# Performance work log

Hardware: AMD Instinct MI355X
Metric: run time of the kernel (lower is better)

The kernel has to match this reference:

```python
import jax, jax.numpy as jnp
import numpy as np

N_NODES = 50000


def gcn_conv(x, src, dst, W, b, n_nodes):
    """PyG GCNConv: add self-loops, sym-normalize, aggregate, linear.
    x' = D^{-1/2} (A + I) D^{-1/2} X W + b
    """
    loop = jnp.arange(n_nodes, dtype=src.dtype)
    s = jnp.concatenate([src, loop])  # [E + N]
    d = jnp.concatenate([dst, loop])
    h = x @ W  # [N, out]
    deg = jax.ops.segment_sum(jnp.ones_like(d, dtype=h.dtype), d, num_segments=n_nodes)
    dinv = jnp.where(deg > 0, jax.lax.rsqrt(deg), 0.0)
    norm = dinv[s] * dinv[d]  # [E + N]
    msg = h[s] * norm[:, None]  # gather + scale (edge-level, memory bound)
    out = jax.ops.segment_sum(msg, d, num_segments=n_nodes)
    return out + b


def setup_inputs() -> dict:
    key = jax.random.key(0)
    k1, k2, k3, k4 = jax.random.split(key, 4)
    n, e, d_in, d_hid, d_out = N_NODES, 800000, 128, 128, 64
    x = jax.random.normal(k1, (n, d_in), dtype=jnp.float32)
    edge_index = jax.random.randint(k2, (2, e), 0, n, dtype=jnp.int64)
    W1 = jax.random.normal(k3, (d_in, d_hid), dtype=jnp.float32) * (1.0 / np.sqrt(d_in))
    b1 = jnp.zeros((d_hid,), dtype=jnp.float32)
    W2 = jax.random.normal(k4, (d_hid, d_out), dtype=jnp.float32) * (1.0 / np.sqrt(d_hid))
    b2 = jnp.zeros((d_out,), dtype=jnp.float32)
    return {"x": x, "edge_index": edge_index, "W1": W1, "b1": b1, "W2": W2, "b2": b2}


def reference(x, edge_index, W1, b1, W2, b2):
    src, dst = edge_index[0], edge_index[1]
    h = gcn_conv(x, src, dst, W1, b1, N_NODES)
    h = jax.nn.relu(h)
    h = gcn_conv(h, src, dst, W2, b2, N_NODES)
    # edge-wise gather + dot product -> per-edge logits [E]
    logits = jnp.sum(h[src] * h[dst], axis=-1)
    return logits
```

## Files before the change

kernel.cpp:

```cpp
#include <hip/hip_runtime.h>
#include <hip/hip_bf16.h>


__global__ void cnt_rank_k(const int* __restrict__ dst, int* __restrict__ cnt,
                           int* __restrict__ rank, int E) {
    int t = blockIdx.x * blockDim.x + threadIdx.x;
    int e = t * 4;
    if (e + 4 <= E) {
        int4 d4 = *reinterpret_cast<const int4*>(dst + e);
        int4 r4;
        r4.x = atomicAdd(&cnt[d4.x], 1);
        r4.y = atomicAdd(&cnt[d4.y], 1);
        r4.z = atomicAdd(&cnt[d4.z], 1);
        r4.w = atomicAdd(&cnt[d4.w], 1);
        *reinterpret_cast<int4*>(rank + e) = r4;
    } else {
        for (int i = e; i < E; i++) rank[i] = atomicAdd(&cnt[dst[i]], 1);
    }
}

__global__ void scan1_k(const int* __restrict__ cnt, int* __restrict__ incl,
                        int* __restrict__ bsum, int N) {
    __shared__ int sh[256];
    int i = blockIdx.x * 256 + threadIdx.x;
    int v = (i < N) ? cnt[i] : 0;
    sh[threadIdx.x] = v;
    __syncthreads();
#pragma unroll
    for (int off = 1; off < 256; off <<= 1) {
        int t = (threadIdx.x >= off) ? sh[threadIdx.x - off] : 0;
        __syncthreads();
        sh[threadIdx.x] += t;
        __syncthreads();
    }
    if (i < N) incl[i] = sh[threadIdx.x];
    if (threadIdx.x == 255) bsum[blockIdx.x] = sh[255];
}

__global__ __launch_bounds__(256) void scan23_k(const int* __restrict__ cnt,
                                                const int* __restrict__ incl,
                                                const int* __restrict__ bsum,
                                                int* __restrict__ rowptr,
                                                float* __restrict__ dinv,
                                                int N, int E, int NB) {
    __shared__ int sh[256];
    __shared__ int blockOff;
    int v = (threadIdx.x < NB) ? bsum[threadIdx.x] : 0;
    sh[threadIdx.x] = v;
    __syncthreads();
#pragma unroll
    for (int off = 1; off < 256; off <<= 1) {
        int t = (threadIdx.x >= off) ? sh[threadIdx.x - off] : 0;
        __syncthreads();
        sh[threadIdx.x] += t;
        __syncthreads();
    }
    if (threadIdx.x == blockIdx.x) blockOff = sh[threadIdx.x] - v;
    __syncthreads();
    int i = blockIdx.x * 256 + threadIdx.x;
    if (i < N) {
        int c = cnt[i];
        rowptr[i] = incl[i] - c + blockOff;
        dinv[i] = rsqrtf(1.0f + (float)c);
    }
    if (i == 0) rowptr[N] = E;
}

template <int BN, bool RELU>
__device__ __forceinline__ void gemm_body32(const float* __restrict__ A,
                                            const float* __restrict__ W,
                                            const float* __restrict__ dscale,
                                            float* __restrict__ Out, int M,
                                            int row0, float (*As)[36],
                                            float (*Bs)[BN]) {
    constexpr int K = 128, BK = 16;
    constexpr int TN = BN / 16;
    const int tid = threadIdx.x;
    const int tx = tid & 15, ty = tid >> 4;

    float acc[2][TN];
#pragma unroll
    for (int m = 0; m < 2; m++)
#pragma unroll
        for (int n = 0; n < TN; n++) acc[m][n] = 0.0f;

    for (int kt = 0; kt < K; kt += BK) {
        if (tid < 128) {
            int r = tid >> 2;
            int kq = (tid & 3) * 4;
            float4 av = make_float4(0.f, 0.f, 0.f, 0.f);
            int gr = row0 + r;
            if (gr < M)
                av = *reinterpret_cast<const float4*>(A + (size_t)gr * K + kt + kq);
            if (RELU) {
                av.x = fmaxf(av.x, 0.f); av.y = fmaxf(av.y, 0.f);
                av.z = fmaxf(av.z, 0.f); av.w = fmaxf(av.w, 0.f);
            }
            As[kq + 0][r] = av.x; As[kq + 1][r] = av.y;
            As[kq + 2][r] = av.z; As[kq + 3][r] = av.w;
        }
#pragma unroll
        for (int s = 0; s < (BK * BN) / (256 * 4); s++) {
            int f = s * 256 + tid;
            int brow = f / (BN / 4);
            int bcol = (f % (BN / 4)) * 4;
            float4 bv = *reinterpret_cast<const float4*>(W + (size_t)(kt + brow) * BN + bcol);
            *reinterpret_cast<float4*>(&Bs[brow][bcol]) = bv;
        }
        __syncthreads();

#pragma unroll
        for (int k = 0; k < BK; k++) {
            float2 a2 = *reinterpret_cast<const float2*>(&As[k][ty * 2]);
            float a[2] = {a2.x, a2.y};
            float b[TN];
            float4 b0 = *reinterpret_cast<const float4*>(&Bs[k][tx * 4]);
            b[0] = b0.x; b[1] = b0.y; b[2] = b0.z; b[3] = b0.w;
            if (TN == 8) {
                float4 b1 = *reinterpret_cast<const float4*>(&Bs[k][64 + tx * 4]);
                b[4] = b1.x; b[5] = b1.y; b[6] = b1.z; b[7] = b1.w;
            }
#pragma unroll
            for (int m = 0; m < 2; m++)
#pragma unroll
                for (int n = 0; n < TN; n++) acc[m][n] = fmaf(a[m], b[n], acc[m][n]);
        }
        __syncthreads();
    }

#pragma unroll
    for (int m = 0; m < 2; m++) {
        int gr = row0 + ty * 2 + m;
        if (gr < M) {
            float dv = dscale[gr];
            float4 o0 = make_float4(acc[m][0] * dv, acc[m][1] * dv,
                                    acc[m][2] * dv, acc[m][3] * dv);
            *reinterpret_cast<float4*>(Out + (size_t)gr * BN + tx * 4) = o0;
            if (TN == 8) {
                float4 o1 = make_float4(acc[m][4] * dv, acc[m][5] * dv,
                                        acc[m][6] * dv, acc[m][7] * dv);
                *reinterpret_cast<float4*>(Out + (size_t)gr * BN + 64 + tx * 4) = o1;
            }
        }
    }
}

__global__ __launch_bounds__(256) void gemm1_fill_k(const float* __restrict__ A,
                                                    const float* __restrict__ W,
                                                    const float* __restrict__ dscale,
                                                    float* __restrict__ Out, int M,
                                                    const int* __restrict__ src,
                                                    const int* __restrict__ dst,
                                                    const int* __restrict__ rowptr,
                                                    const int* __restrict__ rank,
                                                    int2* __restrict__ col2, int E,
                                                    int gemmBlocks) {
    __shared__ float As[16][36];
    __shared__ float Bs[16][128];
    int g = (int)blockIdx.x;
    if (g >= gemmBlocks) {
        int t = (g - gemmBlocks) * 256 + threadIdx.x;
        int e = t * 4;
        if (e + 4 <= E) {
            int4 s4 = *reinterpret_cast<const int4*>(src + e);
            int4 d4 = *reinterpret_cast<const int4*>(dst + e);
            int4 r4 = *reinterpret_cast<const int4*>(rank + e);
            col2[rowptr[d4.x] + r4.x] = make_int2(s4.x, e + 0);
            col2[rowptr[d4.y] + r4.y] = make_int2(s4.y, e + 1);
            col2[rowptr[d4.z] + r4.z] = make_int2(s4.z, e + 2);
            col2[rowptr[d4.w] + r4.w] = make_int2(s4.w, e + 3);
        } else {
            for (int i = e; i < E; i++)
                col2[rowptr[dst[i]] + rank[i]] = make_int2(src[i], i);
        }
        return;
    }
    gemm_body32<128, false>(A, W, dscale, Out, M, g * 32, As, Bs);
}

__global__ __launch_bounds__(256) void gemm2_k(const float* __restrict__ A,
                                               const float* __restrict__ W,
                                               const float* __restrict__ dscale,
                                               float* __restrict__ Out, int M) {
    __shared__ float As[16][36];
    __shared__ float Bs[16][64];
    gemm_body32<64, true>(A, W, dscale, Out, M, (int)blockIdx.x * 32, As, Bs);
}

__global__ __launch_bounds__(256) void pull128_k(const int* __restrict__ rowptr,
                                                 const int2* __restrict__ col2,
                                                 const float4* __restrict__ hs4,
                                                 const float* __restrict__ dinv,
                                                 const float4* __restrict__ bias4,
                                                 float4* __restrict__ out4, int N) {
    int v = (int)((blockIdx.x * (size_t)blockDim.x + threadIdx.x) >> 6);
    if (v >= N) return;
    int lane = threadIdx.x & 63;
    int q = lane & 31, slot = lane >> 5;
    int p0 = rowptr[v], p1 = rowptr[v + 1];

    float4 acc = make_float4(0.f, 0.f, 0.f, 0.f);
    if (slot == 0) acc = hs4[(size_t)v * 32 + q];

    int p = p0;
    for (; p + 8 <= p1; p += 8) {
        int ia = col2[p + slot].x, ib = col2[p + 2 + slot].x;
        int ic = col2[p + 4 + slot].x, id = col2[p + 6 + slot].x;
        float4 a = hs4[(size_t)ia * 32 + q];
        float4 b = hs4[(size_t)ib * 32 + q];
        float4 c = hs4[(size_t)ic * 32 + q];
        float4 d = hs4[(size_t)id * 32 + q];
        acc.x += (a.x + b.x) + (c.x + d.x);
        acc.y += (a.y + b.y) + (c.y + d.y);
        acc.z += (a.z + b.z) + (c.z + d.z);
        acc.w += (a.w + b.w) + (c.w + d.w);
    }
    for (; p + 2 <= p1; p += 2) {
        int ia = col2[p + slot].x;
        float4 a = hs4[(size_t)ia * 32 + q];
        acc.x += a.x; acc.y += a.y; acc.z += a.z; acc.w += a.w;
    }
    if (p < p1 && slot == 0) {
        float4 a = hs4[(size_t)col2[p].x * 32 + q];
        acc.x += a.x; acc.y += a.y; acc.z += a.z; acc.w += a.w;
    }

    acc.x += __shfl_xor(acc.x, 32);
    acc.y += __shfl_xor(acc.y, 32);
    acc.z += __shfl_xor(acc.z, 32);
    acc.w += __shfl_xor(acc.w, 32);

    if (slot == 0) {
        float dv = dinv[v];
        float4 bv = bias4[q];
        out4[(size_t)v * 32 + q] = make_float4(fmaf(acc.x, dv, bv.x), fmaf(acc.y, dv, bv.y),
                                               fmaf(acc.z, dv, bv.z), fmaf(acc.w, dv, bv.w));
    }
}

__global__ __launch_bounds__(256) void pull64_k(const int* __restrict__ rowptr,
                                                const int2* __restrict__ col2,
                                                const float4* __restrict__ hs4,
                                                const float* __restrict__ dinv,
                                                const float4* __restrict__ bias4,
                                                float4* __restrict__ out4, int N) {
    int v = (int)((blockIdx.x * (size_t)blockDim.x + threadIdx.x) >> 6);
    if (v >= N) return;
    int lane = threadIdx.x & 63;
    int q = lane & 15, slot = lane >> 4;
    int p0 = rowptr[v], p1 = rowptr[v + 1];

    float4 acc = make_float4(0.f, 0.f, 0.f, 0.f);
    if (slot == 0) acc = hs4[(size_t)v * 16 + q];

    int p = p0;
    for (; p + 8 <= p1; p += 8) {
        int ia = col2[p + slot].x, ib = col2[p + 4 + slot].x;
        float4 a = hs4[(size_t)ia * 16 + q];
        float4 b = hs4[(size_t)ib * 16 + q];
        acc.x += a.x + b.x; acc.y += a.y + b.y;
        acc.z += a.z + b.z; acc.w += a.w + b.w;
    }
    for (; p + 4 <= p1; p += 4) {
        float4 a = hs4[(size_t)col2[p + slot].x * 16 + q];
        acc.x += a.x; acc.y += a.y; acc.z += a.z; acc.w += a.w;
    }
    int rem = p1 - p;
    if (slot < rem) {
        float4 a = hs4[(size_t)col2[p + slot].x * 16 + q];
        acc.x += a.x; acc.y += a.y; acc.z += a.z; acc.w += a.w;
    }

#pragma unroll
    for (int off = 16; off <= 32; off <<= 1) {
        acc.x += __shfl_xor(acc.x, off);
        acc.y += __shfl_xor(acc.y, off);
        acc.z += __shfl_xor(acc.z, off);
        acc.w += __shfl_xor(acc.w, off);
    }

    if (slot == 0) {
        float dv = dinv[v];
        float4 bv = bias4[q];
        out4[(size_t)v * 16 + q] = make_float4(fmaf(acc.x, dv, bv.x), fmaf(acc.y, dv, bv.y),
                                               fmaf(acc.z, dv, bv.z), fmaf(acc.w, dv, bv.w));
    }
}

__global__ __launch_bounds__(256) void logits_csr_k(const int* __restrict__ rowptr,
                                                    const int2* __restrict__ col2,
                                                    const float4* __restrict__ h4,
                                                    float* __restrict__ out, int N) {
    int v = (int)((blockIdx.x * (size_t)blockDim.x + threadIdx.x) >> 6);
    if (v >= N) return;
    int lane = threadIdx.x & 63;
    int q = lane & 15, slot = lane >> 4;
    int p0 = rowptr[v], p1 = rowptr[v + 1];
    if (p0 == p1) return;

    float4 rd = h4[(size_t)v * 16 + q];

    int p = p0;
    for (; p + 8 <= p1; p += 8) {
        int2 ca = col2[p + slot], cb = col2[p + 4 + slot];
        float4 ra = h4[(size_t)ca.x * 16 + q];
        float4 rb = h4[(size_t)cb.x * 16 + q];
        float t0 = rd.x * ra.x + rd.y * ra.y + rd.z * ra.z + rd.w * ra.w;
        float t1 = rd.x * rb.x + rd.y * rb.y + rd.z * rb.z + rd.w * rb.w;
#pragma unroll
        for (int off = 1; off < 16; off <<= 1) {
            t0 += __shfl_xor(t0, off);
            t1 += __shfl_xor(t1, off);
        }
        if (q == 0) { out[ca.y] = t0; out[cb.y] = t1; }
    }
    for (; p + 4 <= p1; p += 4) {
        int2 ca = col2[p + slot];
        float4 ra = h4[(size_t)ca.x * 16 + q];
        float t0 = rd.x * ra.x + rd.y * ra.y + rd.z * ra.z + rd.w * ra.w;
#pragma unroll
        for (int off = 1; off < 16; off <<= 1) t0 += __shfl_xor(t0, off);
        if (q == 0) out[ca.y] = t0;
    }
    int rem = p1 - p;
    if (slot < rem) {
        int2 ca = col2[p + slot];
        float4 ra = h4[(size_t)ca.x * 16 + q];
        float t0 = rd.x * ra.x + rd.y * ra.y + rd.z * ra.z + rd.w * ra.w;
#pragma unroll
        for (int off = 1; off < 16; off <<= 1) t0 += __shfl_xor(t0, off);
        if (q == 0) out[ca.y] = t0;
    }
}

extern "C" void kernel_launch(void* const* d_in, const int* in_sizes, int n_in,
                              void* d_out, int out_size, void* d_ws, size_t ws_size,
                              hipStream_t stream) {
    const float* x  = (const float*)d_in[0];
    const int* ei   = (const int*)d_in[1];
    const float* W1 = (const float*)d_in[2];
    const float* b1 = (const float*)d_in[3];
    const float* W2 = (const float*)d_in[4];
    const float* b2 = (const float*)d_in[5];
    float* out = (float*)d_out;

    const int N = in_sizes[0] / 128;
    const int E = in_sizes[1] / 2;
    const int* src = ei;
    const int* dst = ei + E;

    float* ws   = (float*)d_ws;
    float* dinv = ws;
    float* bufA = ws + 50176;
    float* bufB = bufA + (size_t)N * 128;
    float* hs1  = bufA;
    float* agg1 = bufB;
    float* g2s  = bufA;
    float* agg2 = bufA + (size_t)N * 64;

    int* ibase  = (int*)(bufB + (size_t)N * 128);
    int* cnt    = ibase;
    int* incl   = cnt + N;
    int* rowptr = incl + N;
    int* bsum   = rowptr + (N + 2);
    int* rank   = bsum + 256;
    int2* col2  = (int2*)(rank + E);

    const int B = 256;
    const int NB = (N + 255) / 256;
    const unsigned nodeBlocks = (unsigned)(((size_t)N * 64 + 255) / 256);

    hipMemsetAsync(cnt, 0, (size_t)N * sizeof(int), stream);
    cnt_rank_k<<<(E / 4 + B - 1) / B, B, 0, stream>>>(dst, cnt, rank, E);
    scan1_k<<<NB, 256, 0, stream>>>(cnt, incl, bsum, N);
    scan23_k<<<NB, 256, 0, stream>>>(cnt, incl, bsum, rowptr, dinv, N, E, NB);

    {
        int gemmBlocks = (N + 31) / 32;
        int fillBlocks = (E / 4 + B - 1) / B;
        gemm1_fill_k<<<gemmBlocks + fillBlocks, 256, 0, stream>>>(
            x, W1, dinv, hs1, N, src, dst, rowptr, rank, col2, E, gemmBlocks);
    }

    pull128_k<<<nodeBlocks, 256, 0, stream>>>(rowptr, col2, (const float4*)hs1, dinv,
                                              (const float4*)b1, (float4*)agg1, N);

    gemm2_k<<<(N + 31) / 32, 256, 0, stream>>>(agg1, W2, dinv, g2s, N);
    pull64_k<<<nodeBlocks, 256, 0, stream>>>(rowptr, col2, (const float4*)g2s, dinv,
                                             (const float4*)b2, (float4*)agg2, N);

    logits_csr_k<<<nodeBlocks, 256, 0, stream>>>(rowptr, col2, (const float4*)agg2, out, N);
}
```

Baseline: 238.4 us.

## Store GEMM outputs in column-chunked layout and split CSR into col/eid arrays

The GEMM epilogues now write their output in a chunked layout: 16-column chunks, each stored contiguously across all nodes. The aggregation kernels are rebuilt so that consecutive blocks handle different column chunks of the same nodes, with each wavefront covering 16 neighbours by 4 float4s. The intent is that each gathered chunk array (about 3.2 MB) stays L2-resident while it is being read, which should raise the gather hit rate. The packed int2 CSR array is split into separate col and eid arrays so the pull kernels read only source indices. The cost is 8x more blocks, each re-reading rowptr and col for the same node, plus scattered GEMM stores.

New measurement: 324.9 us. +36.3%, slower.

```diff
diff --git a/kernel.cpp b/kernel.cpp
--- a/kernel.cpp
+++ b/kernel.cpp
@@ -70,9 +70,9 @@
 __device__ __forceinline__ void gemm_body32(const float* __restrict__ A,
                                             const float* __restrict__ W,
                                             const float* __restrict__ dscale,
-                                            float* __restrict__ Out, int M,
-                                            int row0, float (*As)[36],
-                                            float (*Bs)[BN]) {
+                                            float4* __restrict__ OutT,
+                                            int M, int Nn, int row0,
+                                            float (*As)[36], float (*Bs)[BN]) {
     constexpr int K = 128, BK = 16;
     constexpr int TN = BN / 16;
     const int tid = threadIdx.x;
@@ -128,6 +128,8 @@
         __syncthreads();
     }
 
+    const int chunk0 = tx >> 2;
+    const int off = tx & 3;
 #pragma unroll
     for (int m = 0; m < 2; m++) {
         int gr = row0 + ty * 2 + m;
@@ -135,11 +137,11 @@
             float dv = dscale[gr];
             float4 o0 = make_float4(acc[m][0] * dv, acc[m][1] * dv,
                                     acc[m][2] * dv, acc[m][3] * dv);
-            *reinterpret_cast<float4*>(Out + (size_t)gr * BN + tx * 4) = o0;
+            OutT[((size_t)chunk0 * Nn + gr) * 4 + off] = o0;
             if (TN == 8) {
                 float4 o1 = make_float4(acc[m][4] * dv, acc[m][5] * dv,
                                         acc[m][6] * dv, acc[m][7] * dv);
-                *reinterpret_cast<float4*>(Out + (size_t)gr * BN + 64 + tx * 4) = o1;
+                OutT[((size_t)(4 + chunk0) * Nn + gr) * 4 + off] = o1;
             }
         }
     }
@@ -148,12 +150,14 @@
 __global__ __launch_bounds__(256) void gemm1_fill_k(const float* __restrict__ A,
                                                     const float* __restrict__ W,
                                                     const float* __restrict__ dscale,
-                                                    float* __restrict__ Out, int M,
+                                                    float4* __restrict__ OutT,
+                                                    int M, int Nn,
                                                     const int* __restrict__ src,
                                                     const int* __restrict__ dst,
                                                     const int* __restrict__ rowptr,
                                                     const int* __restrict__ rank,
-                                                    int2* __restrict__ col2, int E,
+                                                    int* __restrict__ col,
+                                                    int* __restrict__ eid, int E,
                                                     int gemmBlocks) {
     __shared__ float As[16][36];
     __shared__ float Bs[16][128];
@@ -165,130 +169,115 @@
             int4 s4 = *reinterpret_cast<const int4*>(src + e);
             int4 d4 = *reinterpret_cast<const int4*>(dst + e);
             int4 r4 = *reinterpret_cast<const int4*>(rank + e);
-            col2[rowptr[d4.x] + r4.x] = make_int2(s4.x, e + 0);
-            col2[rowptr[d4.y] + r4.y] = make_int2(s4.y, e + 1);
-            col2[rowptr[d4.z] + r4.z] = make_int2(s4.z, e + 2);
-            col2[rowptr[d4.w] + r4.w] = make_int2(s4.w, e + 3);
+            int p0 = rowptr[d4.x] + r4.x; col[p0] = s4.x; eid[p0] = e + 0;
+            int p1 = rowptr[d4.y] + r4.y; col[p1] = s4.y; eid[p1] = e + 1;
+            int p2 = rowptr[d4.z] + r4.z; col[p2] = s4.z; eid[p2] = e + 2;
+            int p3 = rowptr[d4.w] + r4.w; col[p3] = s4.w; eid[p3] = e + 3;
         } else {
-            for (int i = e; i < E; i++)
-                col2[rowptr[dst[i]] + rank[i]] = make_int2(src[i], i);
+            for (int i = e; i < E; i++) {
+                int pos = rowptr[dst[i]] + rank[i];
+                col[pos] = src[i]; eid[pos] = i;
+            }
         }
         return;
     }
-    gemm_body32<128, false>(A, W, dscale, Out, M, g * 32, As, Bs);
+    gemm_body32<128, false>(A, W, dscale, OutT, M, Nn, g * 32, As, Bs);
 }
 
 __global__ __launch_bounds__(256) void gemm2_k(const float* __restrict__ A,
                                                const float* __restrict__ W,
                                                const float* __restrict__ dscale,
-                                               float* __restrict__ Out, int M) {
+                                               float4* __restrict__ OutT,
+                                               int M, int Nn) {
     __shared__ float As[16][36];
     __shared__ float Bs[16][64];
-    gemm_body32<64, true>(A, W, dscale, Out, M, (int)blockIdx.x * 32, As, Bs);
-}
-
-__global__ __launch_bounds__(256) void pull128_k(const int* __restrict__ rowptr,
-                                                 const int2* __restrict__ col2,
-                                                 const float4* __restrict__ hs4,
-                                                 const float* __restrict__ dinv,
-                                                 const float4* __restrict__ bias4,
-                                                 float4* __restrict__ out4, int N) {
-    int v = (int)((blockIdx.x * (size_t)blockDim.x + threadIdx.x) >> 6);
+    gemm_body32<64, true>(A, W, dscale, OutT, M, Nn, (int)blockIdx.x * 32, As, Bs);
+}
+
+__global__ __launch_bounds__(256) void pull128c_k(const int* __restrict__ rowptr,
+                                                  const int* __restrict__ col,
+                                                  const float4* __restrict__ hsT,
+                                                  const float* __restrict__ dinv,
+                                                  const float4* __restrict__ bias4,
+                                                  float4* __restrict__ out4, int N) {
+    int c = (int)(blockIdx.x & 7);
+    int k = (int)(blockIdx.x >> 3);
+    int v = k * 4 + (int)(threadIdx.x >> 6);
     if (v >= N) return;
     int lane = threadIdx.x & 63;
-    int q = lane & 31, slot = lane >> 5;
+    int s = lane >> 2, j = lane & 3;
     int p0 = rowptr[v], p1 = rowptr[v + 1];
+    size_t cbase = (size_t)c * N;
 
     float4 acc = make_float4(0.f, 0.f, 0.f, 0.f);
-    if (slot == 0) acc = hs4[(size_t)v * 32 + q];
-
-    int p = p0;
-    for (; p + 8 <= p1; p += 8) {
-        int ia = col2[p + slot].x, ib = col2[p + 2 + slot].x;
-        int ic = col2[p + 4 + slot].x, id = col2[p + 6 + slot].x;
-        float4 a = hs4[(size_t)ia * 32 + q];
-        float4 b = hs4[(size_t)ib * 32 + q];
-        float4 c = hs4[(size_t)ic * 32 + q];
-        float4 d = hs4[(size_t)id * 32 + q];
-        acc.x += (a.x + b.x) + (c.x + d.x);
-        acc.y += (a.y + b.y) + (c.y + d.y);
-        acc.z += (a.z + b.z) + (c.z + d.z);
-        acc.w += (a.w + b.w) + (c.w + d.w);
-    }
-    for (; p + 2 <= p1; p += 2) {
-        int ia = col2[p + slot].x;
-        float4 a = hs4[(size_t)ia * 32 + q];
+    for (int p = p0 + s; p < p1; p += 16) {
+        int u = col[p];
+        float4 a = hsT[(cbase + u) * 4 + j];
         acc.x += a.x; acc.y += a.y; acc.z += a.z; acc.w += a.w;
     }
-    if (p < p1 && slot == 0) {
-        float4 a = hs4[(size_t)col2[p].x * 32 + q];
-        acc.x += a.x; acc.y += a.y; acc.z += a.z; acc.w += a.w;
-    }
-
-    acc.x += __shfl_xor(acc.x, 32);
-    acc.y += __shfl_xor(acc.y, 32);
-    acc.z += __shfl_xor(acc.z, 32);
-    acc.w += __shfl_xor(acc.w, 32);
-
-    if (slot == 0) {
-        float dv = dinv[v];
-        float4 bv = bias4[q];
-        out4[(size_t)v * 32 + q] = make_float4(fmaf(acc.x, dv, bv.x), fmaf(acc.y, dv, bv.y),
-                                               fmaf(acc.z, dv, bv.z), fmaf(acc.w, dv, bv.w));
-    }
-}
-
-__global__ __launch_bounds__(256) void pull64_k(const int* __restrict__ rowptr,
-                                                const int2* __restrict__ col2,
-                                                const float4* __restrict__ hs4,
-                                                const float* __restrict__ dinv,
-                                                const float4* __restrict__ bias4,
-                                                float4* __restrict__ out4, int N) {
-    int v = (int)((blockIdx.x * (size_t)blockDim.x + threadIdx.x) >> 6);
-    if (v >= N) return;
-    int lane = threadIdx.x & 63;
-    int q = lane & 15, slot = lane >> 4;
-    int p0 = rowptr[v], p1 = rowptr[v + 1];
-
-    float4 acc = make_float4(0.f, 0.f, 0.f, 0.f);
-    if (slot == 0) acc = hs4[(size_t)v * 16 + q];
-
-    int p = p0;
-    for (; p + 8 <= p1; p += 8) {
-        int ia = col2[p + slot].x, ib = col2[p + 4 + slot].x;
-        float4 a = hs4[(size_t)ia * 16 + q];
-        float4 b = hs4[(size_t)ib * 16 + q];
-        acc.x += a.x + b.x; acc.y += a.y + b.y;
-        acc.z += a.z + b.z; acc.w += a.w + b.w;
-    }
-    for (; p + 4 <= p1; p += 4) {
-        float4 a = hs4[(size_t)col2[p + slot].x * 16 + q];
-        acc.x += a.x; acc.y += a.y; acc.z += a.z; acc.w += a.w;
-    }
-    int rem = p1 - p;
-    if (slot < rem) {
-        float4 a = hs4[(size_t)col2[p + slot].x * 16 + q];
-        acc.x += a.x; acc.y += a.y; acc.z += a.z; acc.w += a.w;
-    }
-
-#pragma unroll
-    for (int off = 16; off <= 32; off <<= 1) {
+#pragma unroll
+    for (int off = 4; off < 64; off <<= 1) {
         acc.x += __shfl_xor(acc.x, off);
         acc.y += __shfl_xor(acc.y, off);
         acc.z += __shfl_xor(acc.z, off);
         acc.w += __shfl_xor(acc.w, off);
     }
-
-    if (slot == 0) {
+    if (s == 0) {
+        float4 self = hsT[(cbase + v) * 4 + j];
         float dv = dinv[v];
-        float4 bv = bias4[q];
-        out4[(size_t)v * 16 + q] = make_float4(fmaf(acc.x, dv, bv.x), fmaf(acc.y, dv, bv.y),
-                                               fmaf(acc.z, dv, bv.z), fmaf(acc.w, dv, bv.w));
+        float4 bv = bias4[c * 4 + j];
+        float4 o = make_float4(fmaf(acc.x + self.x, dv, bv.x),
+                               fmaf(acc.y + self.y, dv, bv.y),
+                               fmaf(acc.z + self.z, dv, bv.z),
+                               fmaf(acc.w + self.w, dv, bv.w));
+        out4[(size_t)v * 32 + c * 4 + j] = o;
+    }
+}
+
+__global__ __launch_bounds__(256) void pull64c_k(const int* __restrict__ rowptr,
+                                                 const int* __restrict__ col,
+                                                 const float4* __restrict__ g2T,
+                                                 const float* __restrict__ dinv,
+                                                 const float4* __restrict__ bias4,
+                                                 float4* __restrict__ out4, int N) {
+    int m = (int)(blockIdx.x & 7);
+    int c = m & 3;
+    int k = (int)(blockIdx.x >> 3);
+    int v = k * 8 + (m >> 2) * 4 + (int)(threadIdx.x >> 6);
+    if (v >= N) return;
+    int lane = threadIdx.x & 63;
+    int s = lane >> 2, j = lane & 3;
+    int p0 = rowptr[v], p1 = rowptr[v + 1];
+    size_t cbase = (size_t)c * N;
+
+    float4 acc = make_float4(0.f, 0.f, 0.f, 0.f);
+    for (int p = p0 + s; p < p1; p += 16) {
+        int u = col[p];
+        float4 a = g2T[(cbase + u) * 4 + j];
+        acc.x += a.x; acc.y += a.y; acc.z += a.z; acc.w += a.w;
+    }
+#pragma unroll
+    for (int off = 4; off < 64; off <<= 1) {
+        acc.x += __shfl_xor(acc.x, off);
+        acc.y += __shfl_xor(acc.y, off);
+        acc.z += __shfl_xor(acc.z, off);
+        acc.w += __shfl_xor(acc.w, off);
+    }
+    if (s == 0) {
+        float4 self = g2T[(cbase + v) * 4 + j];
+        float dv = dinv[v];
+        float4 bv = bias4[c * 4 + j];
+        float4 o = make_float4(fmaf(acc.x + self.x, dv, bv.x),
+                               fmaf(acc.y + self.y, dv, bv.y),
+                               fmaf(acc.z + self.z, dv, bv.z),
+                               fmaf(acc.w + self.w, dv, bv.w));
+        out4[(size_t)v * 16 + c * 4 + j] = o;
     }
 }
 
 __global__ __launch_bounds__(256) void logits_csr_k(const int* __restrict__ rowptr,
-                                                    const int2* __restrict__ col2,
+                                                    const int* __restrict__ col,
+                                                    const int* __restrict__ eid,
                                                     const float4* __restrict__ h4,
                                                     float* __restrict__ out, int N) {
     int v = (int)((blockIdx.x * (size_t)blockDim.x + threadIdx.x) >> 6);
@@ -302,9 +291,10 @@
 
     int p = p0;
     for (; p + 8 <= p1; p += 8) {
-        int2 ca = col2[p + slot], cb = col2[p + 4 + slot];
-        float4 ra = h4[(size_t)ca.x * 16 + q];
-        float4 rb = h4[(size_t)cb.x * 16 + q];
+        int s0 = col[p + slot], s1 = col[p + 4 + slot];
+        int e0 = eid[p + slot], e1 = eid[p + 4 + slot];
+        float4 ra = h4[(size_t)s0 * 16 + q];
+        float4 rb = h4[(size_t)s1 * 16 + q];
         float t0 = rd.x * ra.x + rd.y * ra.y + rd.z * ra.z + rd.w * ra.w;
         float t1 = rd.x * rb.x + rd.y * rb.y + rd.z * rb.z + rd.w * rb.w;
 #pragma unroll
@@ -312,24 +302,26 @@
             t0 += __shfl_xor(t0, off);
             t1 += __shfl_xor(t1, off);
         }
-        if (q == 0) { out[ca.y] = t0; out[cb.y] = t1; }
+        if (q == 0) { out[e0] = t0; out[e1] = t1; }
     }
     for (; p + 4 <= p1; p += 4) {
-        int2 ca = col2[p + slot];
-        float4 ra = h4[(size_t)ca.x * 16 + q];
+        int s0 = col[p + slot];
+        int e0 = eid[p + slot];
+        float4 ra = h4[(size_t)s0 * 16 + q];
         float t0 = rd.x * ra.x + rd.y * ra.y + rd.z * ra.z + rd.w * ra.w;
 #pragma unroll
         for (int off = 1; off < 16; off <<= 1) t0 += __shfl_xor(t0, off);
-        if (q == 0) out[ca.y] = t0;
+        if (q == 0) out[e0] = t0;
     }
     int rem = p1 - p;
     if (slot < rem) {
-        int2 ca = col2[p + slot];
-        float4 ra = h4[(size_t)ca.x * 16 + q];
+        int s0 = col[p + slot];
+        int e0 = eid[p + slot];
+        float4 ra = h4[(size_t)s0 * 16 + q];
         float t0 = rd.x * ra.x + rd.y * ra.y + rd.z * ra.z + rd.w * ra.w;
 #pragma unroll
         for (int off = 1; off < 16; off <<= 1) t0 += __shfl_xor(t0, off);
-        if (q == 0) out[ca.y] = t0;
+        if (q == 0) out[e0] = t0;
     }
 }
 
@@ -353,18 +345,19 @@
     float* dinv = ws;
     float* bufA = ws + 50176;
     float* bufB = bufA + (size_t)N * 128;
-    float* hs1  = bufA;
+    float* hsT  = bufA;
     float* agg1 = bufB;
-    float* g2s  = bufA;
+    float* g2T  = bufA;
     float* agg2 = bufA + (size_t)N * 64;
 
     int* ibase  = (int*)(bufB + (size_t)N * 128);
     int* cnt    = ibase;
     int* incl   = cnt + N;
     int* rowptr = incl + N;
-    int* bsum   = rowptr + (N + 2);
+    int* bsum   = rowptr + (N + 1);
     int* rank   = bsum + 256;
-    int2* col2  = (int2*)(rank + E);
+    int* col    = rank + E;
+    int* eid    = col + E;
 
     const int B = 256;
     const int NB = (N + 255) / 256;
@@ -379,15 +372,23 @@
         int gemmBlocks = (N + 31) / 32;
         int fillBlocks = (E / 4 + B - 1) / B;
         gemm1_fill_k<<<gemmBlocks + fillBlocks, 256, 0, stream>>>(
-            x, W1, dinv, hs1, N, src, dst, rowptr, rank, col2, E, gemmBlocks);
-    }
-
-    pull128_k<<<nodeBlocks, 256, 0, stream>>>(rowptr, col2, (const float4*)hs1, dinv,
-                                              (const float4*)b1, (float4*)agg1, N);
-
-    gemm2_k<<<(N + 31) / 32, 256, 0, stream>>>(agg1, W2, dinv, g2s, N);
-    pull64_k<<<nodeBlocks, 256, 0, stream>>>(rowptr, col2, (const float4*)g2s, dinv,
-                                             (const float4*)b2, (float4*)agg2, N);
-
-    logits_csr_k<<<nodeBlocks, 256, 0, stream>>>(rowptr, col2, (const float4*)agg2, out, N);
-}
+            x, W1, dinv, (float4*)hsT, N, N, src, dst, rowptr, rank, col, eid, E,
+            gemmBlocks);
+    }
+
+    {
+        unsigned grid = (unsigned)(((N + 3) / 4)) * 8;
+        pull128c_k<<<grid, 256, 0, stream>>>(rowptr, col, (const float4*)hsT, dinv,
+                                             (const float4*)b1, (float4*)agg1, N);
+    }
+
+    gemm2_k<<<(N + 31) / 32, 256, 0, stream>>>(agg1, W2, dinv, (float4*)g2T, N, N);
+
+    {
+        unsigned grid = (unsigned)(((N + 7) / 8)) * 8;
+        pull64c_k<<<grid, 256, 0, stream>>>(rowptr, col, (const float4*)g2T, dinv,
+                                            (const float4*)b2, (float4*)agg2, N);
+    }
+
+    logits_csr_k<<<nodeBlocks, 256, 0, stream>>>(rowptr, col, eid, (const float4*)agg2, out, N);
+}
```
